# Kernel optimization log

Measured on AMD Instinct MI355X. Metric: run time of the kernel, lower is better.

Reference implementation:

```python
import jax, jax.numpy as jnp
import numpy as np
from jax import lax

B, C, H, W = 32, 256, 56, 56
WS = 7            # window size (grid attention: window pixels strided by n1/n2)
NH, DH = 8, 32    # num_head = C // dim_head
EPS = 1e-5        # nn.BatchNorm2d default eps


def _pw(x, w, b):
    # 1x1 conv: (B,C,H,W) x (O,C,1,1) -> (B,O,H,W)
    return jnp.einsum('bchw,oc->bohw', x, w[:, :, 0, 0]) + b[None, :, None, None]


def _dw(x, w, b):
    # depthwise 'same' conv, w: (C,1,k,k)
    k = w.shape[-1]
    p = k // 2
    y = lax.conv_general_dilated(x, w, (1, 1), [(p, p), (p, p)],
                                 dimension_numbers=('NCHW', 'OIHW', 'NCHW'),
                                 feature_group_count=x.shape[1])
    return y + b[None, :, None, None]


def setup_inputs():
    key = jax.random.key(0)
    ks = jax.random.split(key, 8)
    s = 0.05
    return {
        'x': jax.random.normal(ks[0], (B, C, H, W), jnp.float32),
        'bn_gamma': jnp.ones((C,), jnp.float32),
        'bn_beta': jnp.zeros((C,), jnp.float32),
        'qkv_w': jax.random.normal(ks[1], (3 * C, C, 1, 1), jnp.float32) * s,
        'qkv_b': jnp.zeros((3 * C,), jnp.float32),
        'conv3_w': jax.random.normal(ks[2], (C, 1, 3, 3), jnp.float32) * s,
        'conv3_b': jnp.zeros((C,), jnp.float32),
        'conv5_w': jax.random.normal(ks[3], (C, 1, 5, 5), jnp.float32) * s,
        'conv5_b': jnp.zeros((C,), jnp.float32),
        'conv7_w': jax.random.normal(ks[4], (C, 1, 7, 7), jnp.float32) * s,
        'conv7_b': jnp.zeros((C,), jnp.float32),
        'ffn_in_w': jax.random.normal(ks[5], (C, C, 1, 1), jnp.float32) * s,
        'ffn_in_b': jnp.zeros((C,), jnp.float32),
        'conv_local_w': jax.random.normal(ks[6], (C, 1, 3, 3), jnp.float32) * s,
        'conv_local_b': jnp.zeros((C,), jnp.float32),
        'ffn_out_w': jax.random.normal(ks[7], (C, C, 1, 1), jnp.float32) * s,
        'ffn_out_b': jnp.zeros((C,), jnp.float32),
    }


def reference(x, bn_gamma, bn_beta, qkv_w, qkv_b, conv3_w, conv3_b, conv5_w,
              conv5_b, conv7_w, conv7_b, ffn_in_w, ffn_in_b, conv_local_w,
              conv_local_b, ffn_out_w, ffn_out_b):
    # training-mode BatchNorm2d (batch statistics, biased variance)
    mean = x.mean(axis=(0, 2, 3))
    var = x.var(axis=(0, 2, 3))
    xn = bn_gamma[None, :, None, None] * (x - mean[None, :, None, None]) \
         * lax.rsqrt(var + EPS)[None, :, None, None] + bn_beta[None, :, None, None]

    n1, n2 = H // WS, W // WS  # H,W divisible by WS -> pad is a no-op
    # rearrange 'b c (h1 n1) (w1 n2) -> (b n1 n2) c h1 w1' (strided/grid windows)
    xw = xn.reshape(B, C, WS, n1, WS, n2).transpose(0, 3, 5, 1, 2, 4)
    bw = B * n1 * n2
    xw = xw.reshape(bw, C, WS, WS)
    hw = WS * WS

    qkv = _pw(xw, qkv_w, qkv_b)                         # (bw, 3C, WS, WS)
    qkv = qkv.reshape(bw, 3, NH, DH, hw).transpose(1, 0, 2, 4, 3)  # (3,bw,NH,hw,DH)
    q, k, v = qkv[0], qkv[1], qkv[2]
    # v-residual injected before SDPA
    v = v + xw.reshape(bw, NH, DH, hw).transpose(0, 1, 3, 2)

    attn = jax.nn.softmax(jnp.einsum('bnqd,bnkd->bnqk', q, k)
                          / np.float32(np.sqrt(DH)), axis=-1)
    x_spa = jnp.einsum('bnqk,bnkd->bnqd', attn, v)
    x_spa = x_spa.transpose(0, 1, 3, 2).reshape(bw, C, WS, WS)

    # parallel depthwise conv branches, weights all 0.25
    x_spa = 0.25 * (x_spa + _dw(xw, conv3_w, conv3_b)
                    + _dw(xw, conv5_w, conv5_b) + _dw(xw, conv7_w, conv7_b))
    xa = x_spa + v.transpose(0, 1, 3, 2).reshape(bw, C, WS, WS)

    # un-window: '(b n1 n2) c h1 w1 -> b c (h1 n1) (w1 n2)'
    xa = xa.reshape(B, n1, n2, C, WS, WS).transpose(0, 3, 4, 1, 5, 2).reshape(B, C, H, W)

    shortcut = xa
    y = _pw(xa, ffn_in_w, ffn_in_b)
    y = _dw(y, conv_local_w, conv_local_b)
    y = jax.nn.silu(y)
    y = _pw(y, ffn_out_w, ffn_out_b)
    return y + shortcut
```

## Files before the change

### kernel.cpp

```cpp
#include <hip/hip_runtime.h>
#include <hip/hip_bf16.h>

#define NB 32
#define NC 256
#define NHW 3136
#define NA 25690112ull
#define NPW 3328
#define LTS 396

typedef __attribute__((ext_vector_type(8))) short bf16x8;
typedef __attribute__((ext_vector_type(4))) float f32x4;


static __device__ __forceinline__ unsigned short f2bu(float f) {
    union { __hip_bfloat16 h; unsigned short u; } c;
    c.h = __float2bfloat16(f);
    return c.u;
}
static __device__ __forceinline__ float bu2f(unsigned short us) {
    union { unsigned short u; __hip_bfloat16 h; } c;
    c.u = us;
    return __bfloat162float(c.h);
}

__launch_bounds__(256)
__global__ void bn_part(const float* __restrict__ x, float* __restrict__ part)
{
    const int c = blockIdx.x, bq = blockIdx.y;
    const int tid = threadIdx.x;
    float s = 0.f, s2 = 0.f;
    for (int b = bq * 4; b < bq * 4 + 4; ++b) {
        const float4* p = reinterpret_cast<const float4*>(x + ((size_t)b * NC + c) * NHW);
        for (int i = tid; i < 784; i += 256) {
            const float4 v = p[i];
            s += v.x + v.y + v.z + v.w;
            s2 = fmaf(v.x, v.x, s2); s2 = fmaf(v.y, v.y, s2);
            s2 = fmaf(v.z, v.z, s2); s2 = fmaf(v.w, v.w, s2);
        }
    }
    __shared__ float r1[256], r2[256];
    r1[tid] = s; r2[tid] = s2;
    __syncthreads();
    for (int off = 128; off > 0; off >>= 1) {
        if (tid < off) { r1[tid] += r1[tid + off]; r2[tid] += r2[tid + off]; }
        __syncthreads();
    }
    if (tid == 0) {
        part[(c * 8 + bq) * 2] = r1[0];
        part[(c * 8 + bq) * 2 + 1] = r2[0];
    }
}

__launch_bounds__(256)
__global__ void bn_fin(const float* __restrict__ part,
                       const float* __restrict__ gamma, const float* __restrict__ beta,
                       const float* __restrict__ w3, const float* __restrict__ b3,
                       const float* __restrict__ w5, const float* __restrict__ b5,
                       const float* __restrict__ w7, const float* __restrict__ b7,
                       const float* __restrict__ qkvw,
                       const float* __restrict__ fiw, const float* __restrict__ fow,
                       float* __restrict__ ab, float* __restrict__ wcomb,
                       float* __restrict__ bsum, __hip_bfloat16* __restrict__ Wb,
                       __hip_bfloat16* __restrict__ Wfb, __hip_bfloat16* __restrict__ Wob)
{
    const int c = blockIdx.x;
    const int tid = threadIdx.x;

    if (tid < 49) {
        const int ty = tid / 7, tx = tid % 7;
        float wv = w7[c * 49 + tid];
        if (ty >= 1 && ty <= 5 && tx >= 1 && tx <= 5) wv += w5[c * 25 + (ty - 1) * 5 + (tx - 1)];
        if (ty >= 2 && ty <= 4 && tx >= 2 && tx <= 4) wv += w3[c * 9 + (ty - 2) * 3 + (tx - 2)];
        wcomb[c * 49 + tid] = 0.25f * wv;
    }
    if (tid == 63) bsum[c] = 0.25f * (b3[c] + b5[c] + b7[c]);

#pragma unroll
    for (int r = 0; r < 3; ++r) {
        const int o = 3 * c + r;
        Wb[o * 256 + tid] = __float2bfloat16(qkvw[o * 256 + tid]);
    }
    Wfb[c * 256 + tid] = __float2bfloat16(fiw[c * 256 + tid]);
    Wob[c * 256 + tid] = __float2bfloat16(fow[c * 256 + tid]);

    if (tid == 0) {
        float s = 0.f, s2 = 0.f;
#pragma unroll
        for (int q = 0; q < 8; ++q) {
            s += part[(c * 8 + q) * 2];
            s2 += part[(c * 8 + q) * 2 + 1];
        }
        const float inv_n = 1.f / (float)((size_t)NB * NHW);
        const float mean = s * inv_n;
        const float var = s2 * inv_n - mean * mean;
        const float a = gamma[c] / sqrtf(var + 1e-5f);
        ab[c] = a;
        ab[NC + c] = beta[c] - mean * a;
    }
}

__launch_bounds__(256)
__global__ void xnt_make2(const float* __restrict__ x, const float* __restrict__ ab,
                          unsigned short* __restrict__ XNt, unsigned short* __restrict__ XWW)
{
    const int c0 = blockIdx.x * 64;
    const int j1 = blockIdx.y;
    const int b  = blockIdx.z;
    __shared__ unsigned short lt[64 * LTS];
    __shared__ float aa[64], bb[64];
    const int tid = threadIdx.x;
    if (tid < 64) { aa[tid] = ab[c0 + tid]; bb[tid] = ab[256 + c0 + tid]; }
    __syncthreads();

    for (int idx = tid; idx < 6272; idx += 256) {
        const int c = idx / 98, f = idx - 98 * c;
        const int h1 = f / 14, w4 = (f - 14 * h1) * 4;
        const float4 v = *reinterpret_cast<const float4*>(
            &x[((size_t)(b * NC) + c0 + c) * NHW + (h1 * 8 + j1) * 56 + w4]);
        const float a = aa[c], bv = bb[c];
        union { ushort4 u; __hip_bfloat16 h[4]; } pk;
        pk.h[0] = __float2bfloat16(fmaf(a, v.x, bv));
        pk.h[1] = __float2bfloat16(fmaf(a, v.y, bv));
        pk.h[2] = __float2bfloat16(fmaf(a, v.z, bv));
        pk.h[3] = __float2bfloat16(fmaf(a, v.w, bv));
        *reinterpret_cast<ushort4*>(&lt[c * LTS + h1 * 56 + w4]) = pk.u;
    }
    __syncthreads();

    for (int idx = tid; idx < 6656; idx += 256) {
        const int c = idx / 104, r = idx - 104 * c;
        const int j2 = r / 13, q4 = (r - 13 * j2) * 4;
        unsigned short tmp[4];
#pragma unroll
        for (int e = 0; e < 4; ++e) {
            const int p = q4 + e;
            if (p < 49) {
                const int h1p = p / 7, w1 = p - 7 * h1p;
                tmp[e] = lt[c * LTS + h1p * 56 + w1 * 8 + j2];
            } else {
                tmp[e] = 0;
            }
        }
        ushort4 v; v.x = tmp[0]; v.y = tmp[1]; v.z = tmp[2]; v.w = tmp[3];
        *reinterpret_cast<ushort4*>(
            &XWW[((size_t)(b * NC) + c0 + c) * NPW + (j1 * 8 + j2) * 52 + q4]) = v;
    }

    for (int idx = tid; idx < 6272; idx += 256) {
        const int p = idx >> 7;
        const int r = idx & 127;
        const int j2 = r >> 4, c4 = (r & 15) * 4;
        const int h1p = p / 7, w1 = p - 7 * h1p;
        const int px = h1p * 56 + w1 * 8 + j2;
        ushort4 v;
        v.x = lt[(c4 + 0) * LTS + px];
        v.y = lt[(c4 + 1) * LTS + px];
        v.z = lt[(c4 + 2) * LTS + px];
        v.w = lt[(c4 + 3) * LTS + px];
        *reinterpret_cast<ushort4*>(
            &XNt[((size_t)b * NPW + (j1 * 8 + j2) * 52 + p) * 256 + c0 + c4]) = v;
    }
}

__launch_bounds__(256)
__global__ void gemm_qkv_mfma(const unsigned short* __restrict__ XNt,
                              const unsigned short* __restrict__ Wb,
                              const float* __restrict__ bias,
                              unsigned short* __restrict__ QKt,
                              unsigned short* __restrict__ Vb)
{
    __shared__ unsigned short As[128 * 72];
    __shared__ unsigned short Bs[128 * 72];
    const int t = threadIdx.x;
    const int nn0 = blockIdx.x * 128;
    const int o0 = blockIdx.y * 128;
    const int lane = t & 63;
    const int wid = t >> 6;
    const int lr = lane & 15, lg = lane >> 4;
    const int wo = (wid >> 1) * 64;
    const int wn = (wid & 1) * 64;

    f32x4 acc[4][4];
#pragma unroll
    for (int i = 0; i < 4; ++i)
#pragma unroll
        for (int j = 0; j < 4; ++j)
            acc[i][j] = (f32x4){0.f, 0.f, 0.f, 0.f};

    for (int kt = 0; kt < 4; ++kt) {
        const int k0 = kt * 64;
#pragma unroll
        for (int it = 0; it < 4; ++it) {
            const int idx = it * 256 + t;
            const int row = idx >> 3;
            const int k8 = (idx & 7) * 8;
            *reinterpret_cast<uint4*>(&As[row * 72 + k8]) =
                *reinterpret_cast<const uint4*>(&Wb[(size_t)(o0 + row) * 256 + k0 + k8]);
            *reinterpret_cast<uint4*>(&Bs[row * 72 + k8]) =
                *reinterpret_cast<const uint4*>(&XNt[(size_t)(nn0 + row) * 256 + k0 + k8]);
        }
        __syncthreads();
#pragma unroll
        for (int ks = 0; ks < 2; ++ks) {
            const int kk = ks * 32 + lg * 8;
            bf16x8 af[4], bfr[4];
#pragma unroll
            for (int i = 0; i < 4; ++i) {
                af[i]  = *reinterpret_cast<const bf16x8*>(&As[(wo + i * 16 + lr) * 72 + kk]);
                bfr[i] = *reinterpret_cast<const bf16x8*>(&Bs[(wn + i * 16 + lr) * 72 + kk]);
            }
#pragma unroll
            for (int i = 0; i < 4; ++i)
#pragma unroll
                for (int j = 0; j < 4; ++j)
                    acc[i][j] = __builtin_amdgcn_mfma_f32_16x16x32_bf16(
                        af[i], bfr[j], acc[i][j], 0, 0, 0);
        }
        __syncthreads();
    }

    float* Ts = reinterpret_cast<float*>(As);
#pragma unroll
    for (int osub = 0; osub < 4; ++osub) {
        const float4 b4 = *reinterpret_cast<const float4*>(&bias[o0 + wo + osub * 16 + 4 * lg]);
        const int rowb = (wid >> 1) * 16 + 4 * lg;
#pragma unroll
        for (int j = 0; j < 4; ++j) {
            const int col = wn + j * 16 + lr;
            Ts[(rowb + 0) * 132 + col] = acc[osub][j][0] + b4.x;
            Ts[(rowb + 1) * 132 + col] = acc[osub][j][1] + b4.y;
            Ts[(rowb + 2) * 132 + col] = acc[osub][j][2] + b4.z;
            Ts[(rowb + 3) * 132 + col] = acc[osub][j][3] + b4.w;
        }
        __syncthreads();
        if (o0 < 512) {
#pragma unroll
            for (int p = 0; p < 4; ++p) {
                const int item = p * 256 + t;
                const int n = item >> 3;
                const int half = (item >> 2) & 1;
                const int o4 = (item & 3) * 4;
                union { ushort4 u; __hip_bfloat16 h[4]; } pk;
#pragma unroll
                for (int e = 0; e < 4; ++e)
                    pk.h[e] = __float2bfloat16(Ts[(half * 16 + o4 + e) * 132 + n]);
                const int nn = nn0 + n;
                const int bb2 = nn / NPW;
                const int np = nn - bb2 * NPW;
                const int o = o0 + half * 64 + osub * 16 + o4;
                *reinterpret_cast<ushort4*>(&QKt[((size_t)bb2 * NPW + np) * 512 + o]) = pk.u;
            }
        } else {
#pragma unroll
            for (int p = 0; p < 4; ++p) {
                const int idx = p * 256 + t;
                const int row = idx >> 5;
                const int c4 = (idx & 31) * 4;
                const float4 v = *reinterpret_cast<const float4*>(&Ts[row * 132 + c4]);
                const int o = o0 + (row >> 4) * 64 + osub * 16 + (row & 15);
                const int nn = nn0 + c4;
                const int bb2 = nn / NPW;
                const int n = nn - bb2 * NPW;
                union { ushort4 u; __hip_bfloat16 h[4]; } pk;
                pk.h[0] = __float2bfloat16(v.x);
                pk.h[1] = __float2bfloat16(v.y);
                pk.h[2] = __float2bfloat16(v.z);
                pk.h[3] = __float2bfloat16(v.w);
                *reinterpret_cast<ushort4*>(&Vb[((size_t)bb2 * 256 + (o - 512)) * NPW + n]) = pk.u;
            }
        }
        __syncthreads();
    }
}

template<bool RES, bool OUTBF16>
__launch_bounds__(256)
__global__ void gemm_ffn_mfma(const unsigned short* __restrict__ Bt,
                              const unsigned short* __restrict__ Wb2,
                              const float* __restrict__ bias,
                              const float* __restrict__ res, float* __restrict__ outF,
                              unsigned short* __restrict__ outU)
{
    __shared__ unsigned short As[128 * 72];
    __shared__ unsigned short Bs[128 * 72];
    const int t = threadIdx.x;
    const int o0 = blockIdx.x * 128;
    const int nn0 = blockIdx.y * 128;
    const int lane = t & 63;
    const int wid = t >> 6;
    const int lr = lane & 15, lg = lane >> 4;
    const int wo = (wid >> 1) * 64;
    const int wn = (wid & 1) * 64;

    f32x4 acc[4][4];
#pragma unroll
    for (int i = 0; i < 4; ++i)
#pragma unroll
        for (int j = 0; j < 4; ++j)
            acc[i][j] = (f32x4){0.f, 0.f, 0.f, 0.f};

    for (int kt = 0; kt < 4; ++kt) {
        const int k0 = kt * 64;
#pragma unroll
        for (int it = 0; it < 4; ++it) {
            const int idx = it * 256 + t;
            const int row = idx >> 3;
            const int k8 = (idx & 7) * 8;
            *reinterpret_cast<uint4*>(&As[row * 72 + k8]) =
                *reinterpret_cast<const uint4*>(&Wb2[(size_t)(o0 + row) * 256 + k0 + k8]);
            *reinterpret_cast<uint4*>(&Bs[row * 72 + k8]) =
                *reinterpret_cast<const uint4*>(&Bt[(size_t)(nn0 + row) * 256 + k0 + k8]);
        }
        __syncthreads();
#pragma unroll
        for (int ks = 0; ks < 2; ++ks) {
            const int kk = ks * 32 + lg * 8;
            bf16x8 af[4], bfr[4];
#pragma unroll
            for (int i = 0; i < 4; ++i) {
                af[i]  = *reinterpret_cast<const bf16x8*>(&As[(wo + i * 16 + lr) * 72 + kk]);
                bfr[i] = *reinterpret_cast<const bf16x8*>(&Bs[(wn + i * 16 + lr) * 72 + kk]);
            }
#pragma unroll
            for (int i = 0; i < 4; ++i)
#pragma unroll
                for (int j = 0; j < 4; ++j)
                    acc[i][j] = __builtin_amdgcn_mfma_f32_16x16x32_bf16(
                        af[i], bfr[j], acc[i][j], 0, 0, 0);
        }
        __syncthreads();
    }

    float* Ts = reinterpret_cast<float*>(As);
#pragma unroll
    for (int osub = 0; osub < 4; ++osub) {
        const float4 b4 = *reinterpret_cast<const float4*>(&bias[o0 + wo + osub * 16 + 4 * lg]);
        const int rowb = (wid >> 1) * 16 + 4 * lg;
#pragma unroll
        for (int j = 0; j < 4; ++j) {
            const int col = wn + j * 16 + lr;
            Ts[(rowb + 0) * 132 + col] = acc[osub][j][0] + b4.x;
            Ts[(rowb + 1) * 132 + col] = acc[osub][j][1] + b4.y;
            Ts[(rowb + 2) * 132 + col] = acc[osub][j][2] + b4.z;
            Ts[(rowb + 3) * 132 + col] = acc[osub][j][3] + b4.w;
        }
        __syncthreads();
#pragma unroll
        for (int p = 0; p < 4; ++p) {
            const int idx = p * 256 + t;
            const int row = idx >> 5;
            const int c4 = (idx & 31) * 4;
            float4 v = *reinterpret_cast<const float4*>(&Ts[row * 132 + c4]);
            const int o = o0 + (row >> 4) * 64 + osub * 16 + (row & 15);
            const int nn = nn0 + c4;
            const int b2 = nn / NHW;
            const int n = nn - b2 * NHW;
            const size_t po = ((size_t)(b2 * NC + o)) * NHW + n;
            if (OUTBF16) {
                union { ushort4 u; __hip_bfloat16 h[4]; } pk;
                pk.h[0] = __float2bfloat16(v.x);
                pk.h[1] = __float2bfloat16(v.y);
                pk.h[2] = __float2bfloat16(v.z);
                pk.h[3] = __float2bfloat16(v.w);
                *reinterpret_cast<ushort4*>(&outU[po]) = pk.u;
            } else {
                if (RES) {
                    const float4 rv = *reinterpret_cast<const float4*>(&res[po]);
                    v.x += rv.x; v.y += rv.y; v.z += rv.z; v.w += rv.w;
                }
                *reinterpret_cast<float4*>(&outF[po]) = v;
            }
        }
        __syncthreads();
    }
}

__launch_bounds__(64)
__global__ void attn_mfma(const unsigned short* __restrict__ QKt,
                          const unsigned short* __restrict__ Vb,
                          const unsigned short* __restrict__ XWW,
                          const float* __restrict__ wcomb,
                          const float* __restrict__ bsumg,
                          float* __restrict__ xa)
{
    const int j = blockIdx.x;
    const int head = blockIdx.y;
    const int b = blockIdx.z;
    const int c0 = head * 32;
    const int lane = threadIdx.x;
    const int lr = lane & 15, lg = lane >> 4;

    __shared__ __align__(16) char smem[17920];
    unsigned short* P  = (unsigned short*)smem;
    float*          wcl = (float*)smem;
    unsigned short* SP = (unsigned short*)(smem + 6272);
    unsigned short* VT = (unsigned short*)(smem + 10240);
    unsigned short* X  = (unsigned short*)(smem + 14592);

    const size_t qkbase = ((size_t)b * NPW + j * 52) * 512 + c0 + lg * 8;
    uint4 aqr[4], bkr[4];
#pragma unroll
    for (int mi = 0; mi < 4; ++mi) {
        const unsigned short* rp = QKt + qkbase + (size_t)(mi * 16 + lr) * 512;
        aqr[mi] = *reinterpret_cast<const uint4*>(rp);
        bkr[mi] = *reinterpret_cast<const uint4*>(rp + 256);
    }
    const int dd = lane >> 1;
    const int qn = (lane & 1) ? 6 : 7;
    const int qb = (lane & 1) * 7;
    const size_t pbase = ((size_t)(b * NC) + c0 + dd) * NPW + j * 52;
    ushort4 uvr[7], uxr[7];
#pragma unroll
    for (int ii = 0; ii < 7; ++ii)
        if (ii < qn) {
            const int q4 = (qb + ii) * 4;
            uvr[ii] = *reinterpret_cast<const ushort4*>(&Vb[pbase + q4]);
            uxr[ii] = *reinterpret_cast<const ushort4*>(&XWW[pbase + q4]);
        }

    f32x4 acc[4][4];
#pragma unroll
    for (int mi = 0; mi < 4; ++mi)
#pragma unroll
        for (int ni = 0; ni < 4; ++ni)
            acc[mi][ni] = (f32x4){0.f, 0.f, 0.f, 0.f};
    {
        union { uint4 u; bf16x8 v; } ca, cb;
#pragma unroll
        for (int mi = 0; mi < 4; ++mi)
#pragma unroll
            for (int ni = 0; ni < 4; ++ni) {
                ca.u = aqr[mi]; cb.u = bkr[ni];
                acc[mi][ni] = __builtin_amdgcn_mfma_f32_16x16x32_bf16(
                    ca.v, cb.v, acc[mi][ni], 0, 0, 0);
            }
    }

#pragma unroll
    for (int ii = 0; ii < 7; ++ii)
        if (ii < qn) {
            const int q4 = (qb + ii) * 4;
            union { ushort4 u; unsigned short s[4]; } uo;
            const unsigned short* vs = (const unsigned short*)&uvr[ii];
            const unsigned short* xs2 = (const unsigned short*)&uxr[ii];
#pragma unroll
            for (int e = 0; e < 4; ++e) {
                const float vv = bu2f(vs[e]) + bu2f(xs2[e]);
                uo.s[e] = (q4 + e >= 49) ? (unsigned short)0 : f2bu(vv);
            }
            *reinterpret_cast<ushort4*>(&VT[dd * 68 + q4]) = uo.u;
            *reinterpret_cast<ushort4*>(&X[dd * 52 + q4]) = uxr[ii];
        }
    if (lane & 1) {
        ushort4 z; z.x = 0; z.y = 0; z.z = 0; z.w = 0;
        *reinterpret_cast<ushort4*>(&VT[dd * 68 + 52]) = z;
        *reinterpret_cast<ushort4*>(&VT[dd * 68 + 56]) = z;
        *reinterpret_cast<ushort4*>(&VT[dd * 68 + 60]) = z;
    }

    const float sc = 0.17677669529663687f;
#pragma unroll
    for (int mi = 0; mi < 4; ++mi)
#pragma unroll
        for (int reg = 0; reg < 4; ++reg) {
            const float v0 = acc[mi][0][reg] * sc;
            const float v1 = acc[mi][1][reg] * sc;
            const float v2 = acc[mi][2][reg] * sc;
            const float v3 = acc[mi][3][reg] * sc;
            float m = fmaxf(fmaxf(v0, v1), v2);
            if (lr == 0) m = fmaxf(m, v3);
            m = fmaxf(m, __shfl_xor(m, 1));
            m = fmaxf(m, __shfl_xor(m, 2));
            m = fmaxf(m, __shfl_xor(m, 4));
            m = fmaxf(m, __shfl_xor(m, 8));
            const float e0 = __expf(v0 - m), e1 = __expf(v1 - m), e2 = __expf(v2 - m);
            const float e3 = (lr == 0) ? __expf(v3 - m) : 0.f;
            float s = e0 + e1 + e2 + e3;
            s += __shfl_xor(s, 1);
            s += __shfl_xor(s, 2);
            s += __shfl_xor(s, 4);
            s += __shfl_xor(s, 8);
            const float inv = 1.f / s;
            acc[mi][0][reg] = e0 * inv;
            acc[mi][1][reg] = e1 * inv;
            acc[mi][2][reg] = e2 * inv;
            acc[mi][3][reg] = e3 * inv;
        }

#pragma unroll
    for (int mi = 0; mi < 4; ++mi)
#pragma unroll
        for (int ni = 0; ni < 4; ++ni)
#pragma unroll
            for (int reg = 0; reg < 4; ++reg)
                P[(mi * 16 + lg * 4 + reg) * 80 + ni * 16 + lr] = f2bu(acc[mi][ni][reg]);

    f32x4 acc2[4][2];
#pragma unroll
    for (int mi = 0; mi < 4; ++mi)
#pragma unroll
        for (int ni = 0; ni < 2; ++ni)
            acc2[mi][ni] = (f32x4){0.f, 0.f, 0.f, 0.f};
#pragma unroll
    for (int ks = 0; ks < 2; ++ks) {
        bf16x8 ap[4];
#pragma unroll
        for (int mi = 0; mi < 4; ++mi)
            ap[mi] = *reinterpret_cast<const bf16x8*>(&P[(mi * 16 + lr) * 80 + ks * 32 + lg * 8]);
        bf16x8 bv2[2];
#pragma unroll
        for (int ni = 0; ni < 2; ++ni) {
            union { uint2 u[2]; bf16x8 v; } cv;
            cv.u[0] = *reinterpret_cast<const uint2*>(&VT[(ni * 16 + lr) * 68 + ks * 32 + lg * 8]);
            cv.u[1] = *reinterpret_cast<const uint2*>(&VT[(ni * 16 + lr) * 68 + ks * 32 + lg * 8 + 4]);
            bv2[ni] = cv.v;
        }
#pragma unroll
        for (int mi = 0; mi < 4; ++mi)
#pragma unroll
            for (int ni = 0; ni < 2; ++ni)
                acc2[mi][ni] = __builtin_amdgcn_mfma_f32_16x16x32_bf16(
                    ap[mi], bv2[ni], acc2[mi][ni], 0, 0, 0);
    }
    __builtin_amdgcn_sched_barrier(0);

#pragma unroll
    for (int mi = 0; mi < 4; ++mi)
#pragma unroll
        for (int ni = 0; ni < 2; ++ni)
#pragma unroll
            for (int reg = 0; reg < 4; ++reg) {
                const int p = mi * 16 + lg * 4 + reg;
                if (p < 49)
                    SP[(ni * 16 + lr) * 52 + p] = f2bu(acc2[mi][ni][reg]);
            }
    for (int i = lane; i < 392; i += 64)
        *reinterpret_cast<float4*>(&wcl[i * 4]) =
            *reinterpret_cast<const float4*>(&wcomb[c0 * 49 + i * 4]);

    const int j1 = j >> 3, j2 = j & 7;
    for (int it = 0; it < 4; ++it) {
        const int item = it * 64 + lane;
        if (item < 224) {
            const int d = item / 7, h1 = item - 7 * d;
            const float bsv = bsumg[c0 + d];
            float accw[7];
#pragma unroll
            for (int w1 = 0; w1 < 7; ++w1) {
                const int p = h1 * 7 + w1;
                accw[w1] = fmaf(0.25f, bu2f(SP[d * 52 + p]), bsv + bu2f(VT[d * 68 + p]));
            }
#pragma unroll
            for (int dy = 0; dy < 7; ++dy) {
                const int ry = h1 + dy - 3;
                const bool rok = (ry >= 0) && (ry < 7);
                const int ryc = rok ? ry : 0;
                float xr[7];
#pragma unroll
                for (int i2 = 0; i2 < 7; ++i2) {
                    const float xv = bu2f(X[d * 52 + ryc * 7 + i2]);
                    xr[i2] = rok ? xv : 0.f;
                }
#pragma unroll
                for (int dx = 0; dx < 7; ++dx) {
                    const float wv = wcl[d * 49 + dy * 7 + dx];
#pragma unroll
                    for (int w1 = 0; w1 < 7; ++w1) {
                        const int rx = w1 + dx - 3;
                        if (rx >= 0 && rx < 7) accw[w1] = fmaf(wv, xr[rx], accw[w1]);
                    }
                }
            }
            float* xap = xa + ((size_t)(b * NC + c0 + d)) * NHW + (h1 * 8 + j1) * 56 + j2;
#pragma unroll
            for (int w1 = 0; w1 < 7; ++w1) xap[w1 * 8] = accw[w1];
        }
    }
}

template<bool F32IN>
__launch_bounds__(256)
__global__ void t256(const float* __restrict__ srcF, const unsigned short* __restrict__ srcU,
                     unsigned short* __restrict__ dst)
{
    const int n0 = blockIdx.x * 64;
    const int b = blockIdx.y;
    __shared__ unsigned short lt[64 * 264];
    const int t = threadIdx.x;
    for (int idx = t; idx < 4096; idx += 256) {
        const int c = idx >> 4, nq = (idx & 15) * 4;
        ushort4 u;
        if (F32IN) {
            const float4 v = *reinterpret_cast<const float4*>(
                &srcF[((size_t)(b * NC) + c) * NHW + n0 + nq]);
            u.x = f2bu(v.x); u.y = f2bu(v.y); u.z = f2bu(v.z); u.w = f2bu(v.w);
        } else {
            u = *reinterpret_cast<const ushort4*>(
                &srcU[((size_t)(b * NC) + c) * NHW + n0 + nq]);
        }
        lt[(nq + 0) * 264 + c] = u.x;
        lt[(nq + 1) * 264 + c] = u.y;
        lt[(nq + 2) * 264 + c] = u.z;
        lt[(nq + 3) * 264 + c] = u.w;
    }
    __syncthreads();
#pragma unroll
    for (int p = 0; p < 16; ++p) {
        const int idx = p * 256 + t;
        const int row = idx >> 6;
        const int c4 = (idx & 63) * 4;
        *reinterpret_cast<ushort4*>(&dst[((size_t)b * NHW + n0 + row) * 256 + c4]) =
            *reinterpret_cast<const ushort4*>(&lt[row * 264 + c4]);
    }
}

__launch_bounds__(256)
__global__ void dw3_silu(const unsigned short* __restrict__ T, const float* __restrict__ wloc,
                         const float* __restrict__ bloc, unsigned short* __restrict__ Uu)
{
    const int c = blockIdx.x, b = blockIdx.y;
    const size_t pb = ((size_t)b * NC + c) * NHW;
    __shared__ float pl[56 * 57];
    const int tid = threadIdx.x;
    const ushort4* t4 = reinterpret_cast<const ushort4*>(T + pb);
    for (int i = tid; i < 784; i += 256) {
        const ushort4 tv = t4[i];
        const int n = 4 * i;
        const int h = n / 56, w = n - 56 * h;
        pl[h * 57 + w] = bu2f(tv.x);
        pl[h * 57 + w + 1] = bu2f(tv.y);
        pl[h * 57 + w + 2] = bu2f(tv.z);
        pl[h * 57 + w + 3] = bu2f(tv.w);
    }
    __syncthreads();

    float wk[9];
#pragma unroll
    for (int k = 0; k < 9; ++k) wk[k] = wloc[c * 9 + k];
    const float bs = bloc[c];
    unsigned short* up = Uu + pb;
    for (int i4 = tid; i4 < 784; i4 += 256) {
        ushort4 pk;
        unsigned short* pks = (unsigned short*)&pk;
#pragma unroll
        for (int e = 0; e < 4; ++e) {
            const int i = 4 * i4 + e;
            const int h = i / 56, w = i - 56 * h;
            float acc = bs;
#pragma unroll
            for (int dy = -1; dy <= 1; ++dy) {
                const int hh = h + dy;
                if (hh < 0 || hh >= 56) continue;
#pragma unroll
                for (int dx = -1; dx <= 1; ++dx) {
                    const int ww = w + dx;
                    if (ww < 0 || ww >= 56) continue;
                    acc = fmaf(wk[(dy + 1) * 3 + (dx + 1)], pl[hh * 57 + ww], acc);
                }
            }
            pks[e] = f2bu(acc / (1.f + __expf(-acc)));
        }
        *reinterpret_cast<ushort4*>(&up[4 * i4]) = pk;
    }
}

extern "C" void kernel_launch(void* const* d_in, const int* in_sizes, int n_in,
                              void* d_out, int out_size, void* d_ws, size_t ws_size,
                              hipStream_t stream)
{
    (void)in_sizes; (void)n_in; (void)out_size; (void)ws_size;
    const float* x    = (const float*)d_in[0];
    const float* g    = (const float*)d_in[1];
    const float* be   = (const float*)d_in[2];
    const float* qkvw = (const float*)d_in[3];
    const float* qkvb = (const float*)d_in[4];
    const float* w3   = (const float*)d_in[5];
    const float* b3   = (const float*)d_in[6];
    const float* w5   = (const float*)d_in[7];
    const float* b5   = (const float*)d_in[8];
    const float* w7   = (const float*)d_in[9];
    const float* b7   = (const float*)d_in[10];
    const float* fiw  = (const float*)d_in[11];
    const float* fib  = (const float*)d_in[12];
    const float* clw  = (const float*)d_in[13];
    const float* clb  = (const float*)d_in[14];
    const float* fow  = (const float*)d_in[15];
    const float* fob  = (const float*)d_in[16];
    float* out = (float*)d_out;

    float* W     = (float*)d_ws;
    float* ab    = W;
    float* wcomb = W + 512;
    float* bsum  = W + 13056;
    float* part  = W + 13312;
    __hip_bfloat16* Wb  = (__hip_bfloat16*)(W + 17408);
    __hip_bfloat16* Wfb = (__hip_bfloat16*)(W + 115712);
    __hip_bfloat16* Wob = (__hip_bfloat16*)(W + 148480);
    float* xa    = W + 181248;
    unsigned short* XNt = (unsigned short*)xa;
    float* R     = xa + NA;
    unsigned short* QKt = (unsigned short*)R;
    unsigned short* Vb  = QKt + (size_t)NB * NPW * 512;
    unsigned short* XWW = Vb + (size_t)NB * 256 * NPW;
    unsigned short* T   = (unsigned short*)R;
    unsigned short* Uu  = T + NA;
    unsigned short* XAt = Vb;
    unsigned short* Ut  = XWW;

    bn_part<<<dim3(256, 8), dim3(256), 0, stream>>>(x, part);
    bn_fin<<<dim3(256), dim3(256), 0, stream>>>(part, g, be, w3, b3, w5, b5, w7, b7,
                                                qkvw, fiw, fow, ab, wcomb, bsum,
                                                Wb, Wfb, Wob);
    xnt_make2<<<dim3(4, 8, NB), dim3(256), 0, stream>>>(x, ab, XNt, XWW);
    gemm_qkv_mfma<<<dim3(832, 6), dim3(256), 0, stream>>>(
        XNt, (const unsigned short*)Wb, qkvb, QKt, Vb);
    attn_mfma<<<dim3(64, 8, NB), dim3(64), 0, stream>>>(
        QKt, Vb, XWW, wcomb, bsum, xa);
    t256<true><<<dim3(49, NB), dim3(256), 0, stream>>>(xa, nullptr, XAt);
    gemm_ffn_mfma<false, true><<<dim3(2, 784), dim3(256), 0, stream>>>(
        XAt, (const unsigned short*)Wfb, fib, nullptr, nullptr, T);
    dw3_silu<<<dim3(256, NB), dim3(256), 0, stream>>>(T, clw, clb, Uu);
    t256<false><<<dim3(49, NB), dim3(256), 0, stream>>>(nullptr, Uu, Ut);
    gemm_ffn_mfma<true, false><<<dim3(2, 784), dim3(256), 0, stream>>>(
        Ut, (const unsigned short*)Wob, fob, xa, out, nullptr);
}
```

Measured before the change: 834.3 us.

## Store attention output in window-major layout and unpermute inside dw3_silu

The attention kernel now writes xa contiguously in window-major order (j*49 + h1*7 + w1) instead of scattering stride-8 stores into the spatial layout. The FFN pointwise GEMM works per pixel, so it can consume either layout. The dw3_silu kernel then remaps both T and xa back to spatial order through shared memory, and writes xa back in spatial layout for the final residual add. This trades the scattered global writes for an extra full read and write of xa in dw3_silu and more shared memory per block, which may lower occupancy.

```diff
diff --git a/kernel.cpp b/kernel.cpp
--- a/kernel.cpp
+++ b/kernel.cpp
@@ -538,7 +538,6 @@
         *reinterpret_cast<float4*>(&wcl[i * 4]) =
             *reinterpret_cast<const float4*>(&wcomb[c0 * 49 + i * 4]);
 
-    const int j1 = j >> 3, j2 = j & 7;
     for (int it = 0; it < 4; ++it) {
         const int item = it * 64 + lane;
         if (item < 224) {
@@ -571,9 +570,9 @@
                     }
                 }
             }
-            float* xap = xa + ((size_t)(b * NC + c0 + d)) * NHW + (h1 * 8 + j1) * 56 + j2;
-#pragma unroll
-            for (int w1 = 0; w1 < 7; ++w1) xap[w1 * 8] = accw[w1];
+            float* xap = xa + ((size_t)(b * NC + c0 + d)) * NHW + j * 49 + h1 * 7;
+#pragma unroll
+            for (int w1 = 0; w1 < 7; ++w1) xap[w1] = accw[w1];
         }
     }
 }
@@ -616,21 +615,30 @@
 
 __launch_bounds__(256)
 __global__ void dw3_silu(const unsigned short* __restrict__ T, const float* __restrict__ wloc,
-                         const float* __restrict__ bloc, unsigned short* __restrict__ Uu)
+                         const float* __restrict__ bloc, unsigned short* __restrict__ Uu,
+                         float* xa)
 {
     const int c = blockIdx.x, b = blockIdx.y;
     const size_t pb = ((size_t)b * NC + c) * NHW;
     __shared__ float pl[56 * 57];
+    __shared__ float xpl[3136];
     const int tid = threadIdx.x;
     const ushort4* t4 = reinterpret_cast<const ushort4*>(T + pb);
+    const float4* x4 = reinterpret_cast<const float4*>(xa + pb);
     for (int i = tid; i < 784; i += 256) {
         const ushort4 tv = t4[i];
-        const int n = 4 * i;
-        const int h = n / 56, w = n - 56 * h;
-        pl[h * 57 + w] = bu2f(tv.x);
-        pl[h * 57 + w + 1] = bu2f(tv.y);
-        pl[h * 57 + w + 2] = bu2f(tv.z);
-        pl[h * 57 + w + 3] = bu2f(tv.w);
+        const float4 xv = x4[i];
+        const float tt[4] = {bu2f(tv.x), bu2f(tv.y), bu2f(tv.z), bu2f(tv.w)};
+        const float xx[4] = {xv.x, xv.y, xv.z, xv.w};
+#pragma unroll
+        for (int e = 0; e < 4; ++e) {
+            const int n = 4 * i + e;
+            const int j = n / 49, p = n - 49 * j;
+            const int h1 = p / 7, w1 = p - 7 * h1;
+            const int h = h1 * 8 + (j >> 3), w = w1 * 8 + (j & 7);
+            pl[h * 57 + w] = tt[e];
+            xpl[h * 56 + w] = xx[e];
+        }
     }
     __syncthreads();
 
@@ -662,6 +670,10 @@
         }
         *reinterpret_cast<ushort4*>(&up[4 * i4]) = pk;
     }
+
+    float4* xo4 = reinterpret_cast<float4*>(xa + pb);
+    for (int i = tid; i < 784; i += 256)
+        xo4[i] = make_float4(xpl[4 * i], xpl[4 * i + 1], xpl[4 * i + 2], xpl[4 * i + 3]);
 }
 
 extern "C" void kernel_launch(void* const* d_in, const int* in_sizes, int n_in,
@@ -719,7 +731,7 @@
     t256<true><<<dim3(49, NB), dim3(256), 0, stream>>>(xa, nullptr, XAt);
     gemm_ffn_mfma<false, true><<<dim3(2, 784), dim3(256), 0, stream>>>(
         XAt, (const unsigned short*)Wfb, fib, nullptr, nullptr, T);
-    dw3_silu<<<dim3(256, NB), dim3(256), 0, stream>>>(T, clw, clb, Uu);
+    dw3_silu<<<dim3(256, NB), dim3(256), 0, stream>>>(T, clw, clb, Uu, xa);
     t256<false><<<dim3(49, NB), dim3(256), 0, stream>>>(nullptr, Uu, Ut);
     gemm_ffn_mfma<true, false><<<dim3(2, 784), dim3(256), 0, stream>>>(
         Ut, (const unsigned short*)Wob, fob, xa, out, nullptr);
```

New measurement: 792.4 us. 5.0% less time.
